# Optimization experiments

Measured on AMD Instinct MI355X. Metric: run time of the kernel, lower is better.

## Reference

```python
import jax, jax.numpy as jnp
import numpy as np

H = 512   # hidden_size == mm_dim
C = 8     # chunks
R = 8     # rank
S = H // C  # chunk size = 64
OUT = 512 # output_dim of linear_merge
EPS = 1e-12

def _linear(x, w, b):
    # torch nn.Linear convention: w [out, in]
    return x @ w.T + b

def setup_inputs() -> dict:
    key = jax.random.key(0)
    ks = jax.random.split(key, 24)
    B, Lq, Lk, D = 8, 160, 160, 512
    s = 0.02
    inp = {
        'v': jax.random.normal(ks[0], (B, Lk, D), jnp.float32),
        'k': jax.random.normal(ks[1], (B, Lk, D), jnp.float32),
        'q': jax.random.normal(ks[2], (B, Lq, D), jnp.float32),
        # input projections
        'w_v': jax.random.normal(ks[3], (H, D)) * s, 'b_v': jnp.zeros((H,)),
        'w_k': jax.random.normal(ks[4], (H, D)) * s, 'b_k': jnp.zeros((H,)),
        'w_q': jax.random.normal(ks[5], (H, D)) * s, 'b_q': jnp.zeros((H,)),
        # Block: linear0 (applied to key), linear1 (applied to query)
        'w0': jax.random.normal(ks[6], (H, H)) * s, 'b0': jnp.zeros((H,)),
        'w1': jax.random.normal(ks[7], (H, H)) * s, 'b1': jnp.zeros((H,)),
        # per-chunk merge linears, stacked: [C, S*R, S]
        'wm0': jax.random.normal(ks[8], (C, S * R, S)) * s, 'bm0': jnp.zeros((C, S * R)),
        'wm1': jax.random.normal(ks[9], (C, S * R, S)) * s, 'bm1': jnp.zeros((C, S * R)),
        # Block linear_out: mm_dim -> 1
        'w_bo': jax.random.normal(ks[10], (1, H)) * s, 'b_bo': jnp.zeros((1,)),
        # linear_merge: hidden -> output_dim
        'w_m': jax.random.normal(ks[11], (OUT, H)) * s, 'b_m': jnp.zeros((OUT,)),
    }
    return inp

def _block_scores(kx, qx, w0, b0, w1, b1, wm0, bm0, wm1, bm1, w_bo, b_bo):
    # kx: [B,Lk,H] (block arg 0 = key), qx: [B,Lq,H] (block arg 1 = query)
    x0 = _linear(kx, w0, b0)                      # [B,Lk,H]
    x1 = _linear(qx, w1, b1)                      # [B,Lq,H]
    B_, Lk = x0.shape[0], x0.shape[1]
    Lq = x1.shape[1]
    x0c = x0.reshape(B_, Lk, C, S)
    x1c = x1.reshape(B_, Lq, C, S)
    # per-chunk merge projections to rank*size
    y0 = jnp.einsum('bkcs,cts->bkct', x0c, wm0) + bm0  # [B,Lk,C,R*S]
    y1 = jnp.einsum('bqcs,cts->bqct', x1c, wm1) + bm1  # [B,Lq,C,R*S]
    y0 = y0.reshape(B_, Lk, C, R, S)
    y1 = y1.reshape(B_, Lq, C, R, S)
    # elementwise product summed over rank, pairwise over (q,k)
    z = jnp.einsum('bqcrs,bkcrs->bqkcs', y1, y0)  # [B,Lq,Lk,C,S]
    # signed sqrt (power norm) then per-chunk L2 normalize
    z = jnp.sqrt(jax.nn.relu(z)) - jnp.sqrt(jax.nn.relu(-z))
    z = z / jnp.maximum(jnp.linalg.norm(z, axis=-1, keepdims=True), EPS)
    z = z.reshape(B_, Lq, Lk, C * S)
    return _linear(z, w_bo, b_bo).squeeze(-1)     # [B,Lq,Lk]

def reference(v, k, q, w_v, b_v, w_k, b_k, w_q, b_q, w0, b0, w1, b1,
              wm0, bm0, wm1, bm1, w_bo, b_bo, w_m, b_m):
    vv = _linear(v, w_v, b_v)   # [B,Lk,H]
    kk = _linear(k, w_k, b_k)   # [B,Lk,H]
    qq = _linear(q, w_q, b_q)   # [B,Lq,H]
    scores = _block_scores(kk, qq, w0, b0, w1, b1, wm0, bm0, wm1, bm1, w_bo, b_bo)
    att = jax.nn.softmax(scores, axis=-1)          # dropout = identity (eval)
    atted = jnp.einsum('bqk,bkh->bqh', att, vv)    # [B,Lq,H]
    B_ = atted.shape[0]
    # faithful to torch: transpose(1,2).contiguous().view(B,-1,H)
    atted = jnp.swapaxes(atted, 1, 2).reshape(B_, -1, H)
    out = _linear(atted, w_m, b_m)                 # [B,Lq,OUT]
    return jnp.squeeze(out)
```

## Files before the change

### kernel.cpp

```cpp
#include <hip/hip_runtime.h>
#include <hip/hip_bf16.h>

#define B_  8
#define LQ  160
#define LK  160

struct GOps {
    const float* A[3];
    const float* W[3];
    const float* Bi[3];
    float*       C[3];
};

__global__ __launch_bounds__(256) void gemm_f(GOps ops, int K)
{
    const int op = blockIdx.z;
    const float* __restrict__ A  = ops.A[op];
    const float* __restrict__ W  = ops.W[op];
    const float* __restrict__ Bi = ops.Bi[op];
    float* __restrict__       C  = ops.C[op];

    const int m0 = blockIdx.y << 6;
    const int n0 = blockIdx.x << 6;
    const int tid = threadIdx.x;
    const int tm  = tid >> 4;
    const int tn  = tid & 15;
    const int lr  = tid >> 2;
    const int lk4 = (tid & 3) << 2;

    __shared__ float As[16][64];
    __shared__ float Ws[16][64];

    float acc[4][4];
#pragma unroll
    for (int i = 0; i < 4; i++)
#pragma unroll
        for (int j = 0; j < 4; j++) acc[i][j] = 0.f;

    const float* Arow = A + (long)(m0 + lr) * 512 + lk4;
    const float* Wrow = W + (long)(n0 + lr) * K + lk4;
    float4 av = *(const float4*)(Arow);
    float4 wv = *(const float4*)(Wrow);

    for (int k0 = 0; k0 < K; k0 += 16) {
        __syncthreads();
        As[lk4 + 0][lr] = av.x; As[lk4 + 1][lr] = av.y;
        As[lk4 + 2][lr] = av.z; As[lk4 + 3][lr] = av.w;
        Ws[lk4 + 0][lr] = wv.x; Ws[lk4 + 1][lr] = wv.y;
        Ws[lk4 + 2][lr] = wv.z; Ws[lk4 + 3][lr] = wv.w;
        __syncthreads();
        if (k0 + 16 < K) {
            av = *(const float4*)(Arow + k0 + 16);
            wv = *(const float4*)(Wrow + k0 + 16);
        }
#pragma unroll
        for (int kk = 0; kk < 16; kk++) {
            const float4 a4 = *(const float4*)(&As[kk][tm << 2]);
            const float4 b4 = *(const float4*)(&Ws[kk][tn << 2]);
            const float aa[4] = {a4.x, a4.y, a4.z, a4.w};
            const float bb[4] = {b4.x, b4.y, b4.z, b4.w};
#pragma unroll
            for (int i = 0; i < 4; i++)
#pragma unroll
                for (int j = 0; j < 4; j++)
                    acc[i][j] = fmaf(aa[i], bb[j], acc[i][j]);
        }
    }

    const float4 bv = *(const float4*)(Bi + n0 + (tn << 2));
    const float bArr[4] = {bv.x, bv.y, bv.z, bv.w};

#pragma unroll
    for (int i = 0; i < 4; i++) {
        float4 vo;
        vo.x = acc[i][0] + bArr[0]; vo.y = acc[i][1] + bArr[1];
        vo.z = acc[i][2] + bArr[2]; vo.w = acc[i][3] + bArr[3];
        *(float4*)(C + (long)(m0 + (tm << 2) + i) * 512 + n0 + (tn << 2)) = vo;
    }
}

__global__ __launch_bounds__(256) void y_proj(
    const float* __restrict__ x0, const float* __restrict__ wm0, const float* __restrict__ bm0,
    const float* __restrict__ x1, const float* __restrict__ wm1, const float* __restrict__ bm1,
    float* __restrict__ y0t, float* __restrict__ y1p)
{
    const int z   = blockIdx.z;
    const bool is1 = z >= 8;
    const int c   = is1 ? z - 8 : z;
    const float* A  = (is1 ? x1 : x0) + (c << 6);
    const float* W  = (is1 ? wm1 : wm0) + c * 32768;
    const float* Bi = (is1 ? bm1 : bm0) + (c << 9);

    const int m0 = blockIdx.y << 6;
    const int s0 = blockIdx.x << 3;
    const int tid = threadIdx.x;
    const int tm  = tid >> 4;
    const int tn  = tid & 15;
    const int lr  = tid >> 2;
    const int lk4 = (tid & 3) << 2;

    __shared__ float As[16][64];
    __shared__ float Ws[16][64];
    __shared__ float outT[4096];

    float acc[4][4];
#pragma unroll
    for (int i = 0; i < 4; i++)
#pragma unroll
        for (int j = 0; j < 4; j++) acc[i][j] = 0.f;

    const int wrow = ((lr & 7) << 6) + s0 + (lr >> 3);
    const float* Arow = A + (long)(m0 + lr) * 512 + lk4;
    const float* Wrow = W + (long)wrow * 64 + lk4;
    float4 av = *(const float4*)(Arow);
    float4 wv = *(const float4*)(Wrow);

    for (int k0 = 0; k0 < 64; k0 += 16) {
        __syncthreads();
        As[lk4 + 0][lr] = av.x; As[lk4 + 1][lr] = av.y;
        As[lk4 + 2][lr] = av.z; As[lk4 + 3][lr] = av.w;
        Ws[lk4 + 0][lr] = wv.x; Ws[lk4 + 1][lr] = wv.y;
        Ws[lk4 + 2][lr] = wv.z; Ws[lk4 + 3][lr] = wv.w;
        __syncthreads();
        if (k0 + 16 < 64) {
            av = *(const float4*)(Arow + k0 + 16);
            wv = *(const float4*)(Wrow + k0 + 16);
        }
#pragma unroll
        for (int kk = 0; kk < 16; kk++) {
            const float4 a4 = *(const float4*)(&As[kk][tm << 2]);
            const float4 b4 = *(const float4*)(&Ws[kk][tn << 2]);
            const float aa[4] = {a4.x, a4.y, a4.z, a4.w};
            const float bb[4] = {b4.x, b4.y, b4.z, b4.w};
#pragma unroll
            for (int i = 0; i < 4; i++)
#pragma unroll
                for (int j = 0; j < 4; j++)
                    acc[i][j] = fmaf(aa[i], bb[j], acc[i][j]);
        }
    }

    float bArr[4];
#pragma unroll
    for (int j = 0; j < 4; j++) {
        const int ln = (tn << 2) + j;
        bArr[j] = Bi[((ln & 7) << 6) + s0 + (ln >> 3)];
    }
    __syncthreads();
    if (is1) {
#pragma unroll
        for (int i = 0; i < 4; i++) {
            const int m8 = (tm << 2) + i;
#pragma unroll
            for (int j = 0; j < 4; j++) {
                const int ln = (tn << 2) + j;
                outT[(m8 << 6) + ((ln >> 3) << 3) + (ln & 7)] = acc[i][j] + bArr[j];
            }
        }
        __syncthreads();
#pragma unroll
        for (int p = 0; p < 4; p++) {
            const int idx = tid + (p << 8);
            const int m8  = idx >> 4;
            const int f4  = idx & 15;
            *(float4*)(y1p + (long)(m0 + m8) * 4096 + (c << 9) + (s0 << 3) + (f4 << 2))
                = *(const float4*)&outT[idx << 2];
        }
    } else {
#pragma unroll
        for (int i = 0; i < 4; i++) {
            const int k8 = (tm << 2) + i;
#pragma unroll
            for (int j = 0; j < 4; j++) {
                const int ln = (tn << 2) + j;
                outT[((ln >> 3) << 9) + (k8 << 3) + (ln & 7)] = acc[i][j] + bArr[j];
            }
        }
        __syncthreads();
#pragma unroll
        for (int p = 0; p < 4; p++) {
            const int s8  = (p << 1) + (tid >> 7);
            const int u4  = tid & 127;
            const int k8  = u4 >> 1;
            const int r   = (u4 & 1) << 2;
            const int m   = m0 + k8;
            const int bidx = m / 160;
            const int kmod = m - bidx * 160;
            const int s   = s0 + s8;
            float4* dst = (float4*)(y0t +
                (((long)(bidx * 8 + c) * 64 + s) * 160 + kmod) * 8 + r);
            *dst = *(const float4*)&outT[(s8 << 9) + (u4 << 2)];
        }
    }
}

__global__ __launch_bounds__(192) void score_partial(
    const float* __restrict__ y1p, const float* __restrict__ y0t,
    const float* __restrict__ wbo, float* __restrict__ scores_p)
{
    const int id = blockIdx.x;
    const int c  = id & 7;
    const int j  = id >> 3;
    const int b  = j / 40;
    const int q0 = (j - b * 40) << 2;
    const int k  = threadIdx.x;
    const int kc = k < LK ? k : (LK - 1);

    const float* wb = wbo + (c << 6);
    const float* y1r0 = y1p + (long)(b * LQ + q0) * 4096 + (c << 9);
    const float* y1r1 = y1r0 + 4096;
    const float* y1r2 = y1r0 + 8192;
    const float* y1r3 = y1r0 + 12288;
    const float* ybc = y0t + (((long)(b * 8 + c) * 64) * 160 + kc) * 8;

    float num[4] = {0.f, 0.f, 0.f, 0.f};
    float den[4] = {0.f, 0.f, 0.f, 0.f};

    float4 a0 = *(const float4*)(ybc);
    float4 a1 = *(const float4*)(ybc + 4);
#pragma unroll 2
    for (int s = 0; s < 64; s++) {
        const float a[8] = {a0.x, a0.y, a0.z, a0.w, a1.x, a1.y, a1.z, a1.w};
        const int sn = (s + 1) & 63;
        a0 = *(const float4*)(ybc + (long)sn * 1280);
        a1 = *(const float4*)(ybc + (long)sn * 1280 + 4);
        const float w = wb[s];
        const int o = s << 3;
        {
            float zv = a[0] * y1r0[o];
            zv = fmaf(a[1], y1r0[o+1], zv); zv = fmaf(a[2], y1r0[o+2], zv);
            zv = fmaf(a[3], y1r0[o+3], zv); zv = fmaf(a[4], y1r0[o+4], zv);
            zv = fmaf(a[5], y1r0[o+5], zv); zv = fmaf(a[6], y1r0[o+6], zv);
            zv = fmaf(a[7], y1r0[o+7], zv);
            const float az = fabsf(zv);
            num[0] = fmaf(copysignf(__builtin_amdgcn_sqrtf(az), zv), w, num[0]);
            den[0] += az;
        }
        {
            float zv = a[0] * y1r1[o];
            zv = fmaf(a[1], y1r1[o+1], zv); zv = fmaf(a[2], y1r1[o+2], zv);
            zv = fmaf(a[3], y1r1[o+3], zv); zv = fmaf(a[4], y1r1[o+4], zv);
            zv = fmaf(a[5], y1r1[o+5], zv); zv = fmaf(a[6], y1r1[o+6], zv);
            zv = fmaf(a[7], y1r1[o+7], zv);
            const float az = fabsf(zv);
            num[1] = fmaf(copysignf(__builtin_amdgcn_sqrtf(az), zv), w, num[1]);
            den[1] += az;
        }
        {
            float zv = a[0] * y1r2[o];
            zv = fmaf(a[1], y1r2[o+1], zv); zv = fmaf(a[2], y1r2[o+2], zv);
            zv = fmaf(a[3], y1r2[o+3], zv); zv = fmaf(a[4], y1r2[o+4], zv);
            zv = fmaf(a[5], y1r2[o+5], zv); zv = fmaf(a[6], y1r2[o+6], zv);
            zv = fmaf(a[7], y1r2[o+7], zv);
            const float az = fabsf(zv);
            num[2] = fmaf(copysignf(__builtin_amdgcn_sqrtf(az), zv), w, num[2]);
            den[2] += az;
        }
        {
            float zv = a[0] * y1r3[o];
            zv = fmaf(a[1], y1r3[o+1], zv); zv = fmaf(a[2], y1r3[o+2], zv);
            zv = fmaf(a[3], y1r3[o+3], zv); zv = fmaf(a[4], y1r3[o+4], zv);
            zv = fmaf(a[5], y1r3[o+5], zv); zv = fmaf(a[6], y1r3[o+6], zv);
            zv = fmaf(a[7], y1r3[o+7], zv);
            const float az = fabsf(zv);
            num[3] = fmaf(copysignf(__builtin_amdgcn_sqrtf(az), zv), w, num[3]);
            den[3] += az;
        }
    }
    if (k < LK) {
#pragma unroll
        for (int q = 0; q < 4; q++)
            scores_p[(((long)(b * LQ + q0 + q)) * 8 + c) * 160 + k] =
                num[q] / fmaxf(__builtin_amdgcn_sqrtf(den[q]), 1e-12f);
    }
}

__global__ __launch_bounds__(256) void softmax_attv(
    const float* __restrict__ scores_p, const float* __restrict__ vv,
    float* __restrict__ attedT)
{
    const int b  = blockIdx.y;
    const int q0 = blockIdx.x << 2;
    const int tid = threadIdx.x;

    __shared__ float scs[4][160];
    __shared__ float invd[4];

    for (int t = tid; t < 640; t += 256) {
        const int q = t / 160;
        const int k = t - q * 160;
        const float* sp = scores_p + ((long)(b * LQ + q0 + q)) * 1280 + k;
        float s = 0.f;
#pragma unroll
        for (int c = 0; c < 8; c++) s += sp[c * 160];
        scs[q][k] = s;
    }
    __syncthreads();

    const int w    = tid >> 6;
    const int lane = tid & 63;
    {
        const int q = w;
        float m = -1e30f;
        for (int kk = lane; kk < LK; kk += 64) m = fmaxf(m, scs[q][kk]);
#pragma unroll
        for (int off = 32; off; off >>= 1) m = fmaxf(m, __shfl_xor(m, off, 64));
        float sum = 0.f;
        for (int kk = lane; kk < LK; kk += 64) {
            const float e = __expf(scs[q][kk] - m);
            scs[q][kk] = e;
            sum += e;
        }
#pragma unroll
        for (int off = 32; off; off >>= 1) sum += __shfl_xor(sum, off, 64);
        if (lane == 0) invd[q] = 1.f / sum;
    }
    __syncthreads();

    float acc[2][4] = {{0.f,0.f,0.f,0.f},{0.f,0.f,0.f,0.f}};
    const float* vb = vv + (long)b * (LK * 512);
    for (int kk = 0; kk < LK; kk++) {
        const float* vr = vb + kk * 512;
        const float p0 = scs[0][kk], p1 = scs[1][kk];
        const float p2 = scs[2][kk], p3 = scs[3][kk];
        const float v0 = vr[tid], v1 = vr[tid + 256];
        acc[0][0] = fmaf(p0, v0, acc[0][0]); acc[0][1] = fmaf(p1, v0, acc[0][1]);
        acc[0][2] = fmaf(p2, v0, acc[0][2]); acc[0][3] = fmaf(p3, v0, acc[0][3]);
        acc[1][0] = fmaf(p0, v1, acc[1][0]); acc[1][1] = fmaf(p1, v1, acc[1][1]);
        acc[1][2] = fmaf(p2, v1, acc[1][2]); acc[1][3] = fmaf(p3, v1, acc[1][3]);
    }
#pragma unroll
    for (int j = 0; j < 2; j++) {
        const int h = tid + (j << 8);
#pragma unroll
        for (int q = 0; q < 4; q++)
            attedT[((long)b * 512 + h) * 160 + q0 + q] = acc[j][q] * invd[q];
    }
}

extern "C" void kernel_launch(void* const* d_in, const int* in_sizes, int n_in,
                              void* d_out, int out_size, void* d_ws, size_t ws_size,
                              hipStream_t stream) {
    const float* v    = (const float*)d_in[0];
    const float* kin  = (const float*)d_in[1];
    const float* q    = (const float*)d_in[2];
    const float* w_v  = (const float*)d_in[3];
    const float* b_v  = (const float*)d_in[4];
    const float* w_k  = (const float*)d_in[5];
    const float* b_k  = (const float*)d_in[6];
    const float* w_q  = (const float*)d_in[7];
    const float* b_q  = (const float*)d_in[8];
    const float* w0   = (const float*)d_in[9];
    const float* b0   = (const float*)d_in[10];
    const float* w1   = (const float*)d_in[11];
    const float* b1   = (const float*)d_in[12];
    const float* wm0  = (const float*)d_in[13];
    const float* bm0  = (const float*)d_in[14];
    const float* wm1  = (const float*)d_in[15];
    const float* bm1  = (const float*)d_in[16];
    const float* w_bo = (const float*)d_in[17];
    (void)d_in[18];
    const float* w_m  = (const float*)d_in[19];
    const float* b_m  = (const float*)d_in[20];

    float* ws       = (float*)d_ws;
    float* vv       = ws;
    float* kk       = ws + 655360;
    float* qq       = ws + 1310720;
    float* x0       = ws + 1966080;
    float* x1       = ws + 2621440;
    float* y1p      = ws + 3276800;
    float* y0t      = ws + 8519680;
    float* attedT   = ws + 13762560;
    float* scores_p = ws + 655360;

    GOps oA;
    oA.A[0] = v;   oA.W[0] = w_v; oA.Bi[0] = b_v; oA.C[0] = vv;
    oA.A[1] = kin; oA.W[1] = w_k; oA.Bi[1] = b_k; oA.C[1] = kk;
    oA.A[2] = q;   oA.W[2] = w_q; oA.Bi[2] = b_q; oA.C[2] = qq;
    hipLaunchKernelGGL(gemm_f, dim3(8, 20, 3), dim3(256), 0, stream, oA, 512);

    GOps oB;
    oB.A[0] = kk; oB.W[0] = w0; oB.Bi[0] = b0; oB.C[0] = x0;
    oB.A[1] = qq; oB.W[1] = w1; oB.Bi[1] = b1; oB.C[1] = x1;
    oB.A[2] = nullptr; oB.W[2] = nullptr; oB.Bi[2] = nullptr; oB.C[2] = nullptr;
    hipLaunchKernelGGL(gemm_f, dim3(8, 20, 2), dim3(256), 0, stream, oB, 512);

    hipLaunchKernelGGL(y_proj, dim3(8, 20, 16), dim3(256), 0, stream,
                       x0, wm0, bm0, x1, wm1, bm1, y0t, y1p);

    hipLaunchKernelGGL(score_partial, dim3(2560), dim3(192), 0, stream,
                       y1p, y0t, w_bo, scores_p);

    hipLaunchKernelGGL(softmax_attv, dim3(40, 8), dim3(256), 0, stream,
                       scores_p, vv, attedT);

    GOps oF;
    oF.A[0] = attedT; oF.W[0] = w_m; oF.Bi[0] = b_m; oF.C[0] = (float*)d_out;
    oF.A[1] = nullptr; oF.W[1] = nullptr; oF.Bi[1] = nullptr; oF.C[1] = nullptr;
    oF.A[2] = nullptr; oF.W[2] = nullptr; oF.Bi[2] = nullptr; oF.C[2] = nullptr;
    hipLaunchKernelGGL(gemm_f, dim3(8, 20, 1), dim3(256), 0, stream, oF, 512);
}
```

Before: 298.8 us.

## Run k/q projection and block linear GEMMs on bf16 MFMA

Adds a batched fp32-to-bf16 cast kernel for the k/q inputs and four weight matrices, plus a bf16 MFMA GEMM that computes the k/q input projections (writing bf16) and then linear0/linear1 (writing fp32). The v projection stays on the fp32 GEMM. This aims to cut the FP32 GEMM cost for four of the large matmuls by using matrix cores. In exchange it adds a cast launch and extra kernel launches, and bf16 precision loss feeds into the score path. The MFMA kernel reads operands straight from global memory without LDS staging.

```diff
diff --git a/kernel.cpp b/kernel.cpp
--- a/kernel.cpp
+++ b/kernel.cpp
@@ -4,6 +4,80 @@
 #define B_  8
 #define LQ  160
 #define LK  160
+
+typedef __attribute__((ext_vector_type(8))) short bf16x8;
+typedef __attribute__((ext_vector_type(4))) float f32x4;
+
+static __device__ __forceinline__ ushort f2bf(float f) {
+    union { float f; unsigned u; } v; v.f = f;
+    const unsigned r = (v.u + 0x7FFF + ((v.u >> 16) & 1)) >> 16;
+    return (ushort)r;
+}
+
+struct CastArgs { const float4* src[6]; ushort4* dst[6]; int n[6]; };
+
+__global__ __launch_bounds__(256) void cast_bf16k(CastArgs a)
+{
+    const int seg = blockIdx.y;
+    const int i = blockIdx.x * 256 + threadIdx.x;
+    if (i < a.n[seg]) {
+        const float4 v = a.src[seg][i];
+        ushort4 u;
+        u.x = f2bf(v.x); u.y = f2bf(v.y); u.z = f2bf(v.z); u.w = f2bf(v.w);
+        a.dst[seg][i] = u;
+    }
+}
+
+struct MfmaOps { const ushort* A[2]; const ushort* W[2]; const float* Bi[2]; void* C[2]; };
+
+template <int OUTBF>
+__global__ __launch_bounds__(256) void mfma_g(MfmaOps ops)
+{
+    const int op = blockIdx.z;
+    const ushort* __restrict__ A  = ops.A[op];
+    const ushort* __restrict__ W  = ops.W[op];
+    const float*  __restrict__ Bi = ops.Bi[op];
+
+    const int m0 = blockIdx.y << 6;
+    const int n0 = blockIdx.x << 6;
+    const int tid  = threadIdx.x;
+    const int wave = tid >> 6;
+    const int lane = tid & 63;
+    const int l16  = lane & 15;
+    const int kg   = (lane >> 4) << 3;
+
+    const ushort* Ap = A + (long)(m0 + (wave << 4) + l16) * 512 + kg;
+    const ushort* Wp = W + (long)(n0 + l16) * 512 + kg;
+
+    f32x4 acc[4] = {{0.f,0.f,0.f,0.f},{0.f,0.f,0.f,0.f},
+                    {0.f,0.f,0.f,0.f},{0.f,0.f,0.f,0.f}};
+    for (int k0 = 0; k0 < 512; k0 += 32) {
+        const bf16x8 a = *(const bf16x8*)(Ap + k0);
+#pragma unroll
+        for (int nf = 0; nf < 4; nf++) {
+            const bf16x8 b = *(const bf16x8*)(Wp + nf * (16 * 512) + k0);
+            acc[nf] = __builtin_amdgcn_mfma_f32_16x16x32_bf16(a, b, acc[nf], 0, 0, 0);
+        }
+    }
+
+    const int mrow = m0 + (wave << 4) + ((lane >> 4) << 2);
+#pragma unroll
+    for (int nf = 0; nf < 4; nf++) {
+        const int n = n0 + (nf << 4) + l16;
+        const float bias = Bi[n];
+        if (OUTBF) {
+            ushort* C = (ushort*)ops.C[op];
+#pragma unroll
+            for (int r = 0; r < 4; r++)
+                C[(long)(mrow + r) * 512 + n] = f2bf(acc[nf][r] + bias);
+        } else {
+            float* C = (float*)ops.C[op];
+#pragma unroll
+            for (int r = 0; r < 4; r++)
+                C[(long)(mrow + r) * 512 + n] = acc[nf][r] + bias;
+        }
+    }
+}
 
 struct GOps {
     const float* A[3];
@@ -365,26 +439,45 @@
 
     float* ws       = (float*)d_ws;
     float* vv       = ws;
-    float* kk       = ws + 655360;
-    float* qq       = ws + 1310720;
+    ushort* kbf     = (ushort*)(ws + 655360);
+    ushort* qbf     = kbf + 655360;
+    ushort* kkbf    = (ushort*)(ws + 1310720);
+    ushort* qqbf    = kkbf + 655360;
     float* x0       = ws + 1966080;
     float* x1       = ws + 2621440;
     float* y1p      = ws + 3276800;
     float* y0t      = ws + 8519680;
     float* attedT   = ws + 13762560;
+    ushort* wkbf    = (ushort*)(ws + 14417920);
+    ushort* wqbf    = wkbf + 262144;
+    ushort* w0bf    = wkbf + 524288;
+    ushort* w1bf    = wkbf + 786432;
     float* scores_p = ws + 655360;
 
-    GOps oA;
-    oA.A[0] = v;   oA.W[0] = w_v; oA.Bi[0] = b_v; oA.C[0] = vv;
-    oA.A[1] = kin; oA.W[1] = w_k; oA.Bi[1] = b_k; oA.C[1] = kk;
-    oA.A[2] = q;   oA.W[2] = w_q; oA.Bi[2] = b_q; oA.C[2] = qq;
-    hipLaunchKernelGGL(gemm_f, dim3(8, 20, 3), dim3(256), 0, stream, oA, 512);
-
-    GOps oB;
-    oB.A[0] = kk; oB.W[0] = w0; oB.Bi[0] = b0; oB.C[0] = x0;
-    oB.A[1] = qq; oB.W[1] = w1; oB.Bi[1] = b1; oB.C[1] = x1;
-    oB.A[2] = nullptr; oB.W[2] = nullptr; oB.Bi[2] = nullptr; oB.C[2] = nullptr;
-    hipLaunchKernelGGL(gemm_f, dim3(8, 20, 2), dim3(256), 0, stream, oB, 512);
+    CastArgs ca;
+    ca.src[0] = (const float4*)kin; ca.dst[0] = (ushort4*)kbf;  ca.n[0] = 163840;
+    ca.src[1] = (const float4*)q;   ca.dst[1] = (ushort4*)qbf;  ca.n[1] = 163840;
+    ca.src[2] = (const float4*)w_k; ca.dst[2] = (ushort4*)wkbf; ca.n[2] = 65536;
+    ca.src[3] = (const float4*)w_q; ca.dst[3] = (ushort4*)wqbf; ca.n[3] = 65536;
+    ca.src[4] = (const float4*)w0;  ca.dst[4] = (ushort4*)w0bf; ca.n[4] = 65536;
+    ca.src[5] = (const float4*)w1;  ca.dst[5] = (ushort4*)w1bf; ca.n[5] = 65536;
+    hipLaunchKernelGGL(cast_bf16k, dim3(640, 6), dim3(256), 0, stream, ca);
+
+    GOps oV;
+    oV.A[0] = v; oV.W[0] = w_v; oV.Bi[0] = b_v; oV.C[0] = vv;
+    oV.A[1] = oV.A[2] = nullptr; oV.W[1] = oV.W[2] = nullptr;
+    oV.Bi[1] = oV.Bi[2] = nullptr; oV.C[1] = oV.C[2] = nullptr;
+    hipLaunchKernelGGL(gemm_f, dim3(8, 20, 1), dim3(256), 0, stream, oV, 512);
+
+    MfmaOps mA;
+    mA.A[0] = kbf; mA.W[0] = wkbf; mA.Bi[0] = b_k; mA.C[0] = kkbf;
+    mA.A[1] = qbf; mA.W[1] = wqbf; mA.Bi[1] = b_q; mA.C[1] = qqbf;
+    hipLaunchKernelGGL((mfma_g<1>), dim3(8, 20, 2), dim3(256), 0, stream, mA);
+
+    MfmaOps mB;
+    mB.A[0] = kkbf; mB.W[0] = w0bf; mB.Bi[0] = b0; mB.C[0] = x0;
+    mB.A[1] = qqbf; mB.W[1] = w1bf; mB.Bi[1] = b1; mB.C[1] = x1;
+    hipLaunchKernelGGL((mfma_g<0>), dim3(8, 20, 2), dim3(256), 0, stream, mB);
 
     hipLaunchKernelGGL(y_proj, dim3(8, 20, 16), dim3(256), 0, stream,
                        x0, wm0, bm0, x1, wm1, bm1, y0t, y1p);
@@ -397,7 +490,7 @@
 
     GOps oF;
     oF.A[0] = attedT; oF.W[0] = w_m; oF.Bi[0] = b_m; oF.C[0] = (float*)d_out;
-    oF.A[1] = nullptr; oF.W[1] = nullptr; oF.Bi[1] = nullptr; oF.C[1] = nullptr;
-    oF.A[2] = nullptr; oF.W[2] = nullptr; oF.Bi[2] = nullptr; oF.C[2] = nullptr;
+    oF.A[1] = oF.A[2] = nullptr; oF.W[1] = oF.W[2] = nullptr;
+    oF.Bi[1] = oF.Bi[2] = nullptr; oF.C[1] = oF.C[2] = nullptr;
     hipLaunchKernelGGL(gemm_f, dim3(8, 20, 1), dim3(256), 0, stream, oF, 512);
 }
```

New measurement: 298.3 us. About the same (-0.2%).
